# Performance work log

Hardware: AMD Instinct MI355X
Metric: run time of the kernel (lower is better)

The kernel has to match this reference:

```python
import jax, jax.numpy as jnp
import numpy as np

# dims derived from init_kwargs
B, C, T, F = 16, 2, 16, 256
TP, FP = 4, 4            # time/freq patch
MF = F // FP             # 64 freq tokens
TIC = T // TP            # 4 time tokens per chunk
S = MF * TIC             # 256 tokens per chunk
CTX = 3
LEFT = S * CTX           # 768 cached tokens
MT = TIC * (CTX + 1)     # 16 max time positions
D, H, G = 512, 8, 4      # d_model, q heads, kv groups
HD = D // H              # 64
R = H // G               # 2 q-heads per kv group
L = 4                    # layers
FFH = 4 * D
EPS = 1e-5


def _ln(x, g, b):
    m = jnp.mean(x, -1, keepdims=True)
    v = jnp.mean((x - m) ** 2, -1, keepdims=True)
    return (x - m) * jax.lax.rsqrt(v + EPS) * g + b


def setup_inputs() -> dict:
    key = jax.random.key(0)
    ks = iter(jax.random.split(key, 20))
    rn = lambda shape, s=0.05: jax.random.normal(next(ks), shape, jnp.float32) * s
    return {
        "x": rn((B, C, T, F), 1.0),
        "cache_k": rn((L, B, G, LEFT, HD), 1.0),
        "cache_v": rn((L, B, G, LEFT, HD), 1.0),
        "in_W": rn((TP * FP * C, D)), "in_b": jnp.zeros((D,)),
        "ln1_g": jnp.ones((L, D)), "ln1_b": jnp.zeros((L, D)),
        "Wq": rn((L, D, D)), "bq": jnp.zeros((L, D)),
        "Wk": rn((L, D, G * HD)), "bk": jnp.zeros((L, G * HD)),
        "Wv": rn((L, D, G * HD)), "bv": jnp.zeros((L, G * HD)),
        "Wo": rn((L, D, D)), "bo": jnp.zeros((L, D)),
        "rel_time": rn((L, 2 * MT - 1, H)), "rel_freq": rn((L, 2 * MF - 1, H)),
        "res_a": jnp.ones((L,)),
        "ln2_g": jnp.ones((L, D)), "ln2_b": jnp.zeros((L, D)),
        "W1": rn((L, D, FFH)), "b1": jnp.zeros((L, FFH)),
        "W3": rn((L, D, FFH)), "b3": jnp.zeros((L, FFH)),
        "W2": rn((L, FFH, D)), "b2": jnp.zeros((L, D)),
        "res_f": jnp.ones((L,)),
        "out_W": rn((D, TP * FP * C)), "out_b": jnp.zeros((TP * FP * C,)),
    }


def reference(x, cache_k, cache_v, in_W, in_b, ln1_g, ln1_b, Wq, bq, Wk, bk, Wv, bv,
              Wo, bo, rel_time, rel_freq, res_a, ln2_g, ln2_b, W1, b1, W3, b3, W2, b2,
              res_f, out_W, out_b):
    # patchify: (B,C,T,F) -> (B, S, TP*FP*C), token order time-major / freq inner
    h = jnp.transpose(x, (0, 2, 3, 1)).reshape(B, TIC, TP, MF, FP, C)
    h = jnp.transpose(h, (0, 1, 3, 2, 4, 5)).reshape(B, S, TP * FP * C)
    h = h @ in_W + in_b  # (B,S,D)

    # 2D relative position indices (identical each layer)
    K = LEFT + S
    q_idx = jnp.arange(S)
    k_idx = jnp.arange(K)
    qt = LEFT // MF + q_idx // MF  # query time = cache time offset + local time
    qf = q_idx % MF
    kt = k_idx // MF
    kf = k_idx % MF
    dt = qt[:, None] - kt[None, :] + (MT - 1)  # (S,K) in [0, 2*MT-2]
    df = qf[:, None] - kf[None, :] + (MF - 1)  # (S,K) in [0, 2*MF-2]
    scale = 1.0 / np.sqrt(HD).astype(np.float32)

    new_ck, new_cv = [], []
    for l in range(L):
        # --- streaming GQA attention with 2D rel-pos and KV cache ---
        xin = _ln(h, ln1_g[l], ln1_b[l])
        q = (xin @ Wq[l] + bq[l]).reshape(B, S, H, HD)
        k = (xin @ Wk[l] + bk[l]).reshape(B, S, G, HD)
        v = (xin @ Wv[l] + bv[l]).reshape(B, S, G, HD)
        k_full = jnp.concatenate([cache_k[l], jnp.transpose(k, (0, 2, 1, 3))], axis=2)  # (B,G,K,HD)
        v_full = jnp.concatenate([cache_v[l], jnp.transpose(v, (0, 2, 1, 3))], axis=2)
        new_ck.append(k_full[:, :, -LEFT:])
        new_cv.append(v_full[:, :, -LEFT:])
        # group q heads: head h -> group h // R
        scores = jnp.einsum('bsgrd,bgtd->bgrst', q.reshape(B, S, G, R, HD), k_full) * scale
        bias = rel_time[l][dt] + rel_freq[l][df]          # (S,K,H)
        bias = jnp.transpose(bias, (2, 0, 1)).reshape(G, R, S, K)
        attn = jax.nn.softmax(scores + bias[None], axis=-1)
        o = jnp.einsum('bgrst,bgtd->bsgrd', attn, v_full).reshape(B, S, D)
        o = o @ Wo[l] + bo[l]
        h = h + res_a[l] * o  # dropout/droppath identity at eval
        # --- SwiGLU FFN ---
        xin = _ln(h, ln2_g[l], ln2_b[l])
        ff = (jax.nn.silu(xin @ W1[l] + b1[l]) * (xin @ W3[l] + b3[l])) @ W2[l] + b2[l]
        h = h + res_f[l] * ff

    y = h @ out_W + out_b  # (B,S,TP*FP*C)
    # unpatchify back to (B,C,T,F)
    y = y.reshape(B, TIC, MF, TP, FP, C)
    y = jnp.transpose(y, (0, 1, 3, 2, 4, 5)).reshape(B, T, F, C)
    y = jnp.transpose(y, (0, 3, 1, 2))
    return y, jnp.stack(new_ck), jnp.stack(new_cv)
```

## Files before the change

kernel.cpp:

```cpp
#include <hip/hip_runtime.h>
#include <stdint.h>

typedef __attribute__((ext_vector_type(8))) short bf16x8;
typedef __attribute__((ext_vector_type(4))) float f32x4;

#define B_    16
#define S_    256
#define LEFT_ 768
#define KT_   1024
#define D_    512
#define H_    8
#define G_    4
#define HD_   64
#define L_    4
#define FFH_  2048
#define M_    4096
#define LOG2E 1.44269504f

__device__ __forceinline__ unsigned short f2b(float f){
  unsigned u = __float_as_uint(f);
  u += 0x7fffu + ((u>>16)&1u);
  return (unsigned short)(u>>16);
}

__device__ __forceinline__ unsigned cvt_pk_bf16(float lo, float hi){
  unsigned r;
  asm("v_cvt_pk_bf16_f32 %0, %1, %2" : "=v"(r) : "v"(lo), "v"(hi));
  return r;
}

__device__ __forceinline__ void gl_lds16(const unsigned short* g, void* l){
  __builtin_amdgcn_global_load_lds(
    (const __attribute__((address_space(1))) unsigned int*)g,
    (__attribute__((address_space(3))) unsigned int*)l, 16, 0, 0);
}

template<int BM, int BN, int WM, int WN, class BRowF>
__device__ __forceinline__ void mfma_core(
    const unsigned short* Abase, int lda, int m0, BRowF brow,
    int kd, char* As, char* Bs, f32x4* acc)
{
  constexpr int FR = WM/16, FC = WN/16;
  constexpr int NWC = BN/WN;
  constexpr int CA = BM/64, CB = BN/64;
  const int tid = threadIdx.x, wave = tid>>6, lane = tid&63;
  const int wr = wave / NWC, wc = wave % NWC;
  const int lr = lane>>2;
  const int swl = (lane&3) ^ ((lane>>2)&3) ^ (lane>>4);

  auto stage = [&](int buf, int k0){
    #pragma unroll
    for (int i = 0; i < CA; ++i) {
      const int chunk = wave*CA + i;
      const unsigned short* gp = Abase + (size_t)(m0 + chunk*16 + lr)*lda + k0 + swl*8;
      gl_lds16(gp, As + buf*(BM*64) + chunk*1024);
    }
    #pragma unroll
    for (int i = 0; i < CB; ++i) {
      const int chunk = wave*CB + i;
      const unsigned short* gp = brow(chunk*16 + lr) + k0 + swl*8;
      gl_lds16(gp, Bs + buf*(BN*64) + chunk*1024);
    }
  };

  stage(0, 0);
  __syncthreads();
  int cur = 0;
  for (int k0 = 0; k0 < kd; k0 += 32) {
    if (k0 + 32 < kd) stage(cur^1, k0 + 32);
    bf16x8 af[FR], bfr[FC];
    #pragma unroll
    for (int r = 0; r < FR; ++r)
      af[r] = *(const bf16x8*)(As + cur*(BM*64) + (wr*WM + r*16 + (lane&15))*64 + swl*16);
    #pragma unroll
    for (int c = 0; c < FC; ++c)
      bfr[c] = *(const bf16x8*)(Bs + cur*(BN*64) + (wc*WN + c*16 + (lane&15))*64 + swl*16);
    #pragma unroll
    for (int r = 0; r < FR; ++r)
      #pragma unroll
      for (int c = 0; c < FC; ++c)
        acc[r*FC+c] = __builtin_amdgcn_mfma_f32_16x16x32_bf16(af[r], bfr[c], acc[r*FC+c], 0, 0, 0);
    __syncthreads();
    cur ^= 1;
  }
}

__device__ __forceinline__ void tcvt_body(
    const float* __restrict__ src, unsigned short* __restrict__ dst,
    int K, int N, int ntk, int ntn, int bx)
{
  __shared__ float t[64][65];
  int kt = bx % ntk; int nt = (bx/ntk) % ntn; int l = bx/(ntk*ntn);
  src += (size_t)l*K*N; dst += (size_t)l*N*K;
  const int k0 = kt*64, n0 = nt*64;
  const int tid = threadIdx.x;
  #pragma unroll
  for (int i = 0; i < 4; ++i) {
    int kr = (tid>>4) + i*16;
    const float4 v = *(const float4*)&src[(size_t)(k0+kr)*N + n0 + (tid&15)*4];
    t[kr][(tid&15)*4+0]=v.x; t[kr][(tid&15)*4+1]=v.y;
    t[kr][(tid&15)*4+2]=v.z; t[kr][(tid&15)*4+3]=v.w;
  }
  __syncthreads();
  const int nn = tid>>2, kk = (tid&3)*16;
  unsigned w[8];
  #pragma unroll
  for (int j = 0; j < 8; ++j)
    w[j] = (unsigned)f2b(t[kk+2*j][nn]) | ((unsigned)f2b(t[kk+2*j+1][nn])<<16);
  size_t off = (size_t)(n0+nn)*K + k0 + kk;
  *(uint4*)&dst[off]     = make_uint4(w[0],w[1],w[2],w[3]);
  *(uint4*)&dst[off + 8] = make_uint4(w[4],w[5],w[6],w[7]);
}

__global__ __launch_bounds__(256) void transpose_all(
    const float* __restrict__ Wq, const float* __restrict__ Wk,
    const float* __restrict__ Wv, const float* __restrict__ Wo,
    const float* __restrict__ W1, const float* __restrict__ W3,
    const float* __restrict__ W2,
    unsigned short* __restrict__ Wqt, unsigned short* __restrict__ Wkt,
    unsigned short* __restrict__ Wvt, unsigned short* __restrict__ Wot,
    unsigned short* __restrict__ W1t, unsigned short* __restrict__ W3t,
    unsigned short* __restrict__ W2t)
{
  int bx = blockIdx.x;
  if      (bx < 256)  tcvt_body(Wq, Wqt, 512, 512, 8, 8,  bx);
  else if (bx < 384)  tcvt_body(Wk, Wkt, 512, 256, 8, 4,  bx-256);
  else if (bx < 512)  tcvt_body(Wv, Wvt, 512, 256, 8, 4,  bx-384);
  else if (bx < 768)  tcvt_body(Wo, Wot, 512, 512, 8, 8,  bx-512);
  else if (bx < 1792) tcvt_body(W1, W1t, 512, 2048, 8, 32, bx-768);
  else if (bx < 2816) tcvt_body(W3, W3t, 512, 2048, 8, 32, bx-1792);
  else                tcvt_body(W2, W2t, 2048, 512, 32, 8, bx-2816);
}

__global__ __launch_bounds__(256) void patchify_inproj(
    const float* __restrict__ x, const float* __restrict__ inW,
    const float* __restrict__ inb, float* __restrict__ h)
{
  int bs = blockIdx.x;
  int b = bs >> 8, s = bs & 255;
  int tic = s >> 6, mf = s & 63;
  __shared__ float ps[32];
  int tid = threadIdx.x;
  if (tid < 32) {
    int tp = tid >> 3, fp = (tid >> 1) & 3, c = tid & 1;
    ps[tid] = x[((size_t)(b*2 + c)*16 + tic*4 + tp)*256 + mf*4 + fp];
  }
  __syncthreads();
  #pragma unroll
  for (int rep = 0; rep < 2; ++rep) {
    int d = tid + rep*256;
    float acc = inb[d];
    #pragma unroll
    for (int i = 0; i < 32; ++i) acc += ps[i] * inW[i*D_ + d];
    h[(size_t)bs*D_ + d] = acc;
  }
}

__global__ __launch_bounds__(256) void ln_stats(
    const float* __restrict__ h, float* __restrict__ smean, float* __restrict__ srstd)
{
  const int tid = threadIdx.x;
  const int row = blockIdx.x*16 + (tid>>4);
  const int qd = tid & 15;
  const float* rp = h + (size_t)row*512 + qd*32;
  float s = 0.f, sq = 0.f;
  #pragma unroll
  for (int i = 0; i < 8; ++i) {
    float4 v = ((const float4*)rp)[i];
    s  += (v.x+v.y)+(v.z+v.w);
    sq += (v.x*v.x+v.y*v.y)+(v.z*v.z+v.w*v.w);
  }
  #pragma unroll
  for (int o = 1; o < 16; o <<= 1) { s += __shfl_xor(s,o,64); sq += __shfl_xor(sq,o,64); }
  if (qd == 0) {
    float mean = s*(1.f/512.f);
    smean[row] = mean;
    srstd[row] = rsqrtf(sq*(1.f/512.f) - mean*mean + 1e-5f);
  }
}

__global__ __launch_bounds__(256) void ln_kernel(
    const float* __restrict__ in, unsigned short* __restrict__ out,
    const float* __restrict__ g, const float* __restrict__ bta)
{
  const int tid = threadIdx.x;
  const int row = blockIdx.x*16 + (tid>>4);
  const int qd = tid & 15;
  const float* rp = in + (size_t)row*512 + qd*32;
  float4 xv[8];
  float s = 0.f, sq = 0.f;
  #pragma unroll
  for (int i = 0; i < 8; ++i) {
    xv[i] = ((const float4*)rp)[i];
    s  += (xv[i].x+xv[i].y)+(xv[i].z+xv[i].w);
    sq += (xv[i].x*xv[i].x + xv[i].y*xv[i].y)+(xv[i].z*xv[i].z + xv[i].w*xv[i].w);
  }
  #pragma unroll
  for (int o = 1; o < 16; o <<= 1) { s += __shfl_xor(s,o,64); sq += __shfl_xor(sq,o,64); }
  const float mean = s*(1.f/512.f);
  const float rstd = rsqrtf(sq*(1.f/512.f) - mean*mean + 1e-5f);
  const float* gp = g + qd*32;
  const float* bp = bta + qd*32;
  unsigned short* op = out + (size_t)row*512 + qd*32;
  #pragma unroll
  for (int i = 0; i < 4; ++i) {
    float4 a  = xv[2*i],                 b2 = xv[2*i+1];
    float4 ga = ((const float4*)gp)[2*i], gb = ((const float4*)gp)[2*i+1];
    float4 ba = ((const float4*)bp)[2*i], bb = ((const float4*)bp)[2*i+1];
    unsigned w0 = (unsigned)f2b((a.x-mean)*rstd*ga.x + ba.x) | ((unsigned)f2b((a.y-mean)*rstd*ga.y + ba.y)<<16);
    unsigned w1 = (unsigned)f2b((a.z-mean)*rstd*ga.z + ba.z) | ((unsigned)f2b((a.w-mean)*rstd*ga.w + ba.w)<<16);
    unsigned w2 = (unsigned)f2b((b2.x-mean)*rstd*gb.x + bb.x) | ((unsigned)f2b((b2.y-mean)*rstd*gb.y + bb.y)<<16);
    unsigned w3 = (unsigned)f2b((b2.z-mean)*rstd*gb.z + bb.z) | ((unsigned)f2b((b2.w-mean)*rstd*gb.w + bb.w)<<16);
    *(uint4*)(op + i*8) = make_uint4(w0,w1,w2,w3);
  }
}

__global__ __launch_bounds__(256) void qkv_ln_gemm(
    const float* __restrict__ h,
    const float* __restrict__ smean, const float* __restrict__ srstd,
    const float* __restrict__ lng, const float* __restrict__ lnb,
    const unsigned short* __restrict__ Wqt, const unsigned short* __restrict__ Wkt,
    const unsigned short* __restrict__ Wvt,
    const float* __restrict__ bq, const float* __restrict__ bk_, const float* __restrict__ bv_,
    unsigned short* __restrict__ q_bf, unsigned short* __restrict__ kf_bf,
    unsigned short* __restrict__ vnew, float* __restrict__ nck, float* __restrict__ ncv)
{
  __shared__ alignas(16) char As[2][64*64];
  __shared__ alignas(16) char Bs[2][128*64];
  int bx = (blockIdx.x & 7)*64 + (blockIdx.x >> 3);
  const int mt = bx >> 3, nt = bx & 7;
  const int m0 = mt*64, n0 = nt*128;
  const int tid = threadIdx.x, wave = tid>>6, lane = tid&63;

  const int ar = tid >> 2, au = tid & 3;
  const int ap = au ^ (ar&3) ^ ((ar>>2)&3);
  const float* arow = h + (size_t)(m0 + ar)*512;
  const float mean_r = smean[m0 + ar];
  const float rstd_r = srstd[m0 + ar];

  const int lr = lane>>2;
  const int swl = (lane&3) ^ ((lane>>2)&3) ^ (lane>>4);
  auto brow = [&](int rr) -> const unsigned short* {
    int n = n0 + rr;
    return n < 512 ? Wqt + (size_t)n*512
         : n < 768 ? Wkt + (size_t)(n-512)*512
                   : Wvt + (size_t)(n-768)*512;
  };
  auto stageB = [&](int buf, int k0){
    #pragma unroll
    for (int i = 0; i < 2; ++i) {
      const int chunk = wave*2 + i;
      gl_lds16(brow(chunk*16+lr) + k0 + swl*8, (char*)Bs[buf] + chunk*1024);
    }
  };

  float4 av[6];
  auto loadA = [&](int k0){
    av[0] = *(const float4*)(arow + k0 + au*8);
    av[1] = *(const float4*)(arow + k0 + au*8 + 4);
    av[2] = *(const float4*)(lng  + k0 + au*8);
    av[3] = *(const float4*)(lng  + k0 + au*8 + 4);
    av[4] = *(const float4*)(lnb  + k0 + au*8);
    av[5] = *(const float4*)(lnb  + k0 + au*8 + 4);
  };
  auto writeA = [&](int buf){
    const float* xv = (const float*)&av[0];
    const float* gv = (const float*)&av[2];
    const float* bv2 = (const float*)&av[4];
    unsigned w[4];
    #pragma unroll
    for (int j = 0; j < 4; ++j) {
      float e0 = (xv[2*j]   - mean_r)*rstd_r*gv[2*j]   + bv2[2*j];
      float e1 = (xv[2*j+1] - mean_r)*rstd_r*gv[2*j+1] + bv2[2*j+1];
      w[j] = (unsigned)f2b(e0) | ((unsigned)f2b(e1)<<16);
    }
    *(uint4*)((char*)As[buf] + ar*64 + ap*16) = make_uint4(w[0],w[1],w[2],w[3]);
  };

  loadA(0);
  stageB(0, 0);
  writeA(0);
  __syncthreads();

  f32x4 acc[8] = {};
  const int wr = wave >> 1, wc = wave & 1;
  for (int k0 = 0; k0 < 512; k0 += 32) {
    const int cur = (k0>>5)&1;
    const bool more = (k0 + 32 < 512);
    if (more) { stageB(cur^1, k0+32); loadA(k0+32); }
    bf16x8 af[2], bfv[4];
    #pragma unroll
    for (int r = 0; r < 2; ++r)
      af[r] = *(const bf16x8*)((char*)As[cur] + (wr*32 + r*16 + (lane&15))*64 + swl*16);
    #pragma unroll
    for (int c = 0; c < 4; ++c)
      bfv[c] = *(const bf16x8*)((char*)Bs[cur] + (wc*64 + c*16 + (lane&15))*64 + swl*16);
    #pragma unroll
    for (int r = 0; r < 2; ++r)
      #pragma unroll
      for (int c = 0; c < 4; ++c)
        acc[r*4+c] = __builtin_amdgcn_mfma_f32_16x16x32_bf16(af[r], bfv[c], acc[r*4+c], 0,0,0);
    if (more) writeA(cur^1);
    __syncthreads();
  }

  #pragma unroll
  for (int r = 0; r < 2; ++r)
  #pragma unroll
  for (int c = 0; c < 4; ++c) {
    f32x4 v = acc[r*4+c];
    #pragma unroll
    for (int reg = 0; reg < 4; ++reg) {
      int m = m0 + wr*32 + r*16 + ((lane>>4)<<2) + reg;
      int n = n0 + wc*64 + c*16 + (lane&15);
      float val = v[reg];
      int b = m >> 8, s = m & 255;
      if (n < 512) {
        q_bf[(size_t)m*512 + n] = f2b(val + bq[n]);
      } else if (n < 768) {
        int g = (n-512) >> 6, hd = n & 63;
        float kv = val + bk_[n-512];
        kf_bf[((size_t)(b*4+g)*1024 + 768 + s)*64 + hd] = f2b(kv);
        nck [((size_t)(b*4+g)*768  + 512 + s)*64 + hd] = kv;
      } else {
        int g = (n-768) >> 6, hd = n & 63;
        float vv = val + bv_[n-768];
        vnew[(size_t)m*256 + (n-768)] = f2b(vv);
        ncv [((size_t)(b*4+g)*768 + 512 + s)*64 + hd] = vv;
      }
    }
  }
}

__global__ __launch_bounds__(256) void merge_kv(
    const float* __restrict__ ck, const float* __restrict__ cv,
    const unsigned short* __restrict__ vnew,
    unsigned short* __restrict__ kf_bf, unsigned short* __restrict__ vt_bf,
    float* __restrict__ nck, float* __restrict__ ncv)
{
  __shared__ float t[64][65];
  const int bb = blockIdx.x;
  const int tid = threadIdx.x;
  if (bb < 3072) {
    size_t idx = (size_t)bb*256 + tid;
    int hd4 = idx & 15;
    size_t tt = (idx >> 4) % 768;
    size_t bg = idx / (16*768);
    const float4 v = ((const float4*)ck)[idx];
    uint2 pk;
    pk.x = (unsigned)f2b(v.x) | ((unsigned)f2b(v.y)<<16);
    pk.y = (unsigned)f2b(v.z) | ((unsigned)f2b(v.w)<<16);
    *(uint2*)&kf_bf[((bg*1024 + tt)*64) + hd4*4] = pk;
    if (tt >= 256)
      ((float4*)nck)[(bg*768 + (tt-256))*16 + hd4] = v;
  } else if (bb < 3840) {
    const int bi = bb - 3072;
    const int bg = bi / 12, tt = bi % 12;
    const int t0 = tt*64;
    #pragma unroll
    for (int i = 0; i < 4; ++i) {
      int tr = (tid>>4) + i*16;
      const float4 v = ((const float4*)cv)[((size_t)bg*768 + t0+tr)*16 + (tid&15)];
      t[tr][(tid&15)*4+0]=v.x; t[tr][(tid&15)*4+1]=v.y;
      t[tr][(tid&15)*4+2]=v.z; t[tr][(tid&15)*4+3]=v.w;
      if (t0+tr >= 256)
        ((float4*)ncv)[((size_t)bg*768 + t0+tr-256)*16 + (tid&15)] = v;
    }
    __syncthreads();
    const int hd = tid>>2, tc = (tid&3)*16;
    unsigned w[8];
    #pragma unroll
    for (int j = 0; j < 8; ++j)
      w[j] = (unsigned)f2b(t[tc+2*j][hd]) | ((unsigned)f2b(t[tc+2*j+1][hd])<<16);
    size_t off = ((size_t)bg*64 + hd)*1024 + t0 + tc;
    *(uint4*)&vt_bf[off]     = make_uint4(w[0],w[1],w[2],w[3]);
    *(uint4*)&vt_bf[off + 8] = make_uint4(w[4],w[5],w[6],w[7]);
  } else {
    const int bi = bb - 3840;
    const int bg = bi >> 2, tt4 = bi & 3;
    const int b = bg >> 2, g = bg & 3;
    const int t0 = 768 + tt4*64;
    unsigned short* ts = (unsigned short*)&t[0][0];
    #pragma unroll
    for (int i = 0; i < 4; ++i) {
      int tr = (tid>>4) + i*16;
      uint2 v = *(const uint2*)&vnew[((size_t)(b*256 + (t0-768) + tr))*256 + g*64 + (tid&15)*4];
      const unsigned short* pv4 = (const unsigned short*)&v;
      ts[tr*68 + (tid&15)*4 + 0] = pv4[0];
      ts[tr*68 + (tid&15)*4 + 1] = pv4[1];
      ts[tr*68 + (tid&15)*4 + 2] = pv4[2];
      ts[tr*68 + (tid&15)*4 + 3] = pv4[3];
    }
    __syncthreads();
    const int hd = tid>>2, tc = (tid&3)*16;
    unsigned w[8];
    #pragma unroll
    for (int j = 0; j < 8; ++j)
      w[j] = (unsigned)ts[(tc+2*j)*68 + hd] | ((unsigned)ts[(tc+2*j+1)*68 + hd] << 16);
    size_t off = ((size_t)bg*64 + hd)*1024 + t0 + tc;
    *(uint4*)&vt_bf[off]     = make_uint4(w[0],w[1],w[2],w[3]);
    *(uint4*)&vt_bf[off + 8] = make_uint4(w[4],w[5],w[6],w[7]);
  }
}

__global__ __launch_bounds__(512) void flash_attn(
    const unsigned short* __restrict__ q_bf,
    const unsigned short* __restrict__ kf_bf,
    const unsigned short* __restrict__ vt_bf,
    const float* __restrict__ relt,
    const float* __restrict__ relf,
    unsigned short* __restrict__ att_bf)
{
  int bx = (blockIdx.x & 7)*32 + (blockIdx.x >> 3);
  const int qt = bx & 1, hh = (bx>>1) & 7, b = bx >> 4;
  const int g = hh >> 1;
  const int tid = threadIdx.x, wave = tid>>6, lane = tid&63;
  const int lg = lane>>4, lq = lane&15;
  const int qloc = wave*16 + lq;
  const int q0 = qt*128;
  const int qtg = qt*2 + (wave>>2);

  __shared__ alignas(16) char Ks[2][16384];
  __shared__ alignas(16) char Vs[2][16384];

  const unsigned short* kfb  = kf_bf + (size_t)(b*4+g)*1024*64;
  const unsigned short* vtb2 = vt_bf + (size_t)(b*4+g)*64*1024;

  auto stage = [&](int buf, int t){
    #pragma unroll
    for (int it = 0; it < 2; ++it) {
      int slot = it*512 + tid;
      int kr = slot>>3, kp = slot&7,  ku = kp ^ (kr&7);
      gl_lds16(kfb + (size_t)(t*128 + kr)*64 + ku*8, Ks[buf] + slot*16);
      int vr = slot>>4, vp = slot&15, vu = vp ^ (vr&15);
      gl_lds16(vtb2 + (size_t)vr*1024 + t*128 + vu*8, Vs[buf] + slot*16);
    }
  };

  const unsigned short* qrow = q_bf + ((size_t)(b*256 + q0 + qloc))*512 + hh*64;
  bf16x8 qfrag[2];
  qfrag[0] = *(const bf16x8*)(qrow + lg*8);
  qfrag[1] = *(const bf16x8*)(qrow + 32 + lg*8);

  float bias_f[4][4];
  {
    int sq = qloc & 63;
    #pragma unroll
    for (int f = 0; f < 4; ++f)
      #pragma unroll
      for (int r = 0; r < 4; ++r)
        bias_f[f][r] = relf[((sq - (f*16 + lg*4 + r)) + 63)*8 + hh] * LOG2E;
  }
  const float scale2 = 0.125f * LOG2E;

  f32x4 ot[4] = {};
  float m_run = -1e30f, l_part = 0.f;

  stage(0, 0);
  __syncthreads();

  for (int t = 0; t < 8; ++t) {
    const int cur = t & 1;
    if (t + 1 < 8) stage(cur^1, t+1);

    f32x4 st[8] = {};
    __builtin_amdgcn_s_setprio(1);
    #pragma unroll
    for (int c = 0; c < 2; ++c)
      #pragma unroll
      for (int f = 0; f < 8; ++f) {
        int row = f*16 + lq;
        int pu = (c*4 + lg) ^ (row & 7);
        bf16x8 kf_ = *(const bf16x8*)(Ks[cur] + row*128 + pu*16);
        st[f] = __builtin_amdgcn_mfma_f32_16x16x32_bf16(kf_, qfrag[c], st[f], 0,0,0);
      }
    __builtin_amdgcn_s_setprio(0);

    const float bt0 = relt[(27 + qtg - 2*t)*8 + hh] * LOG2E;
    const float bt1 = relt[(27 + qtg - 2*t - 1)*8 + hh] * LOG2E;
    float mt = -1e30f;
    #pragma unroll
    for (int f = 0; f < 8; ++f) {
      const float bt = (f < 4) ? bt0 : bt1;
      #pragma unroll
      for (int r = 0; r < 4; ++r) {
        float v = st[f][r]*scale2 + bt + bias_f[f&3][r];
        st[f][r] = v;
        mt = fmaxf(mt, v);
      }
    }
    mt = fmaxf(mt, __shfl_xor(mt, 16, 64));
    mt = fmaxf(mt, __shfl_xor(mt, 32, 64));
    if (!__all(mt - m_run <= 11.5416f)) {
      const float m_new = fmaxf(m_run, mt);
      const float corr = exp2f(m_run - m_new);
      m_run = m_new;
      l_part *= corr;
      #pragma unroll
      for (int f = 0; f < 4; ++f) {
        ot[f][0] *= corr; ot[f][1] *= corr; ot[f][2] *= corr; ot[f][3] *= corr;
      }
    }
    float psum = 0.f;
    unsigned r01[8], r23[8];
    #pragma unroll
    for (int f = 0; f < 8; ++f) {
      float e0 = exp2f(st[f][0] - m_run);
      float e1 = exp2f(st[f][1] - m_run);
      float e2 = exp2f(st[f][2] - m_run);
      float e3 = exp2f(st[f][3] - m_run);
      psum += (e0+e1)+(e2+e3);
      r01[f] = cvt_pk_bf16(e0, e1);
      r23[f] = cvt_pk_bf16(e2, e3);
    }
    l_part += psum;

    const int src0 = (lg&1)*32 + lq;
    const int src1 = src0 + 16;
    const bool hi = (lg>>1) != 0;
    #pragma unroll
    for (int c = 0; c < 4; ++c) {
      unsigned a0 = (unsigned)__shfl((int)r01[c*2],   src0, 64);
      unsigned b0 = (unsigned)__shfl((int)r01[c*2+1], src0, 64);
      unsigned a1 = (unsigned)__shfl((int)r23[c*2],   src0, 64);
      unsigned b1 = (unsigned)__shfl((int)r23[c*2+1], src0, 64);
      unsigned a2 = (unsigned)__shfl((int)r01[c*2],   src1, 64);
      unsigned b2 = (unsigned)__shfl((int)r01[c*2+1], src1, 64);
      unsigned a3 = (unsigned)__shfl((int)r23[c*2],   src1, 64);
      unsigned b3 = (unsigned)__shfl((int)r23[c*2+1], src1, 64);
      uint4 bw;
      bw.x = hi ? b0 : a0;
      bw.y = hi ? b1 : a1;
      bw.z = hi ? b2 : a2;
      bw.w = hi ? b3 : a3;
      bf16x8 pfrag = *(bf16x8*)&bw;
      __builtin_amdgcn_s_setprio(1);
      #pragma unroll
      for (int f = 0; f < 4; ++f) {
        int row = f*16 + lq;
        int pu = (c*4 + lg) ^ (row & 15);
        bf16x8 vf_ = *(const bf16x8*)(Vs[cur] + row*256 + pu*16);
        ot[f] = __builtin_amdgcn_mfma_f32_16x16x32_bf16(vf_, pfrag, ot[f], 0,0,0);
      }
      __builtin_amdgcn_s_setprio(0);
    }
    __syncthreads();
  }

  float l_tot = l_part + __shfl_xor(l_part, 16, 64);
  l_tot += __shfl_xor(l_tot, 32, 64);
  const float inv = 1.0f / l_tot;
  unsigned short* orow = att_bf + ((size_t)(b*256 + q0 + qloc))*512 + hh*64;
  #pragma unroll
  for (int f = 0; f < 4; ++f) {
    uint2 w;
    w.x = (unsigned)f2b(ot[f][0]*inv) | ((unsigned)f2b(ot[f][1]*inv)<<16);
    w.y = (unsigned)f2b(ot[f][2]*inv) | ((unsigned)f2b(ot[f][3]*inv)<<16);
    *(uint2*)(orow + f*16 + lg*4) = w;
  }
}

__global__ __launch_bounds__(256) void ffn1_gemm(
    const unsigned short* __restrict__ xin,
    const unsigned short* __restrict__ W1t, const unsigned short* __restrict__ W3t,
    const float* __restrict__ b1_, const float* __restrict__ b3_,
    unsigned short* __restrict__ ff_bf)
{
  __shared__ alignas(16) char As[2*128*64];
  __shared__ alignas(16) char Bs[2*128*64];
  f32x4 acc[16] = {};
  int bx = (blockIdx.x & 7)*128 + (blockIdx.x >> 3);
  const int nt = bx & 31, mt = bx >> 5;
  const int m0 = mt*128, n0 = nt*128;
  auto brow = [&](int r) -> const unsigned short* {
    int p = n0 + r;
    int pb = p >> 4;
    int j = ((pb>>1)<<4) | (p & 15);
    return (pb & 1) ? W3t + (size_t)j*512 : W1t + (size_t)j*512;
  };
  mfma_core<128,128,64,64>(xin, 512, m0, brow, 512, As, Bs, acc);
  const int lane = threadIdx.x & 63, wave = threadIdx.x >> 6;
  const int wr = wave >> 1, wc = wave & 1;
  #pragma unroll
  for (int r = 0; r < 4; ++r)
  #pragma unroll
  for (int cp = 0; cp < 4; cp += 2) {
    f32x4 va = acc[r*4+cp];
    f32x4 vb = acc[r*4+cp+1];
    #pragma unroll
    for (int reg = 0; reg < 4; ++reg) {
      int m = m0 + wr*64 + r*16 + ((lane>>4)<<2) + reg;
      int p = n0 + wc*64 + cp*16 + (lane&15);
      int j = ((p>>5)<<4) | (p & 15);
      float a = va[reg] + b1_[j];
      float bb = vb[reg] + b3_[j];
      float gval = (a / (1.0f + __expf(-a))) * bb;
      ff_bf[(size_t)m*2048 + j] = f2b(gval);
    }
  }
}

__global__ __launch_bounds__(256) void res_gemm(
    const unsigned short* __restrict__ A, int lda,
    const unsigned short* __restrict__ Wt, int kd,
    const float* __restrict__ bias, const float* __restrict__ resv,
    float* __restrict__ h)
{
  __shared__ alignas(16) char As[2*64*64];
  __shared__ alignas(16) char Bs[2*64*64];
  f32x4 acc[4] = {};
  int bx = (blockIdx.x & 7)*64 + (blockIdx.x >> 3);
  const int mt = bx >> 3, nt = bx & 7;
  const int m0 = mt*64, n0 = nt*64;
  auto brow = [&](int r) -> const unsigned short* {
    return Wt + (size_t)(n0 + r)*kd;
  };
  mfma_core<64,64,32,32>(A, lda, m0, brow, kd, As, Bs, acc);
  const float rv = resv[0];
  const int lane = threadIdx.x & 63, wave = threadIdx.x >> 6;
  const int wr = wave >> 1, wc = wave & 1;
  #pragma unroll
  for (int r = 0; r < 2; ++r)
  #pragma unroll
  for (int c = 0; c < 2; ++c) {
    f32x4 v = acc[r*2+c];
    #pragma unroll
    for (int reg = 0; reg < 4; ++reg) {
      int m = m0 + wr*32 + r*16 + ((lane>>4)<<2) + reg;
      int n = n0 + wc*32 + c*16 + (lane&15);
      h[(size_t)m*512 + n] += rv * (v[reg] + bias[n]);
    }
  }
}

__global__ __launch_bounds__(256) void outproj_kernel(
    const float* __restrict__ h, const float* __restrict__ outW,
    const float* __restrict__ outb, float* __restrict__ y)
{
  int bs = blockIdx.x;
  int b = bs >> 8, s = bs & 255;
  int tic = s >> 6, mf = s & 63;
  __shared__ float hr[512];
  __shared__ float part[8][32];
  int tid = threadIdx.x;
  hr[tid]     = h[(size_t)bs*D_ + tid];
  hr[tid+256] = h[(size_t)bs*D_ + tid + 256];
  __syncthreads();
  int i = tid & 31, seg = tid >> 5;
  float acc = 0.0f;
  #pragma unroll
  for (int k = 0; k < 64; ++k) acc += hr[seg*64 + k] * outW[(seg*64 + k)*32 + i];
  part[seg][i] = acc;
  __syncthreads();
  if (tid < 32) {
    float v = outb[tid];
    #pragma unroll
    for (int s2 = 0; s2 < 8; ++s2) v += part[s2][tid];
    int tp = tid >> 3, fp = (tid >> 1) & 3, c = tid & 1;
    y[((size_t)(b*2 + c)*16 + tic*4 + tp)*256 + mf*4 + fp] = v;
  }
}

extern "C" void kernel_launch(void* const* d_in, const int* in_sizes, int n_in,
                              void* d_out, int out_size, void* d_ws, size_t ws_size,
                              hipStream_t stream) {
  (void)in_sizes; (void)n_in; (void)out_size; (void)ws_size;
  const float* x        = (const float*)d_in[0];
  const float* cache_k  = (const float*)d_in[1];
  const float* cache_v  = (const float*)d_in[2];
  const float* in_W     = (const float*)d_in[3];
  const float* in_b     = (const float*)d_in[4];
  const float* ln1_g    = (const float*)d_in[5];
  const float* ln1_b    = (const float*)d_in[6];
  const float* Wq       = (const float*)d_in[7];
  const float* bq       = (const float*)d_in[8];
  const float* Wk       = (const float*)d_in[9];
  const float* bk       = (const float*)d_in[10];
  const float* Wv       = (const float*)d_in[11];
  const float* bv       = (const float*)d_in[12];
  const float* Wo       = (const float*)d_in[13];
  const float* bo       = (const float*)d_in[14];
  const float* rel_time = (const float*)d_in[15];
  const float* rel_freq = (const float*)d_in[16];
  const float* res_a    = (const float*)d_in[17];
  const float* ln2_g    = (const float*)d_in[18];
  const float* ln2_b    = (const float*)d_in[19];
  const float* W1       = (const float*)d_in[20];
  const float* b1       = (const float*)d_in[21];
  const float* W3       = (const float*)d_in[22];
  const float* b3       = (const float*)d_in[23];
  const float* W2       = (const float*)d_in[24];
  const float* b2       = (const float*)d_in[25];
  const float* res_f    = (const float*)d_in[26];
  const float* out_W    = (const float*)d_in[27];
  const float* out_b    = (const float*)d_in[28];

  char* ws = (char*)d_ws;
  size_t o = 0;
  float* h            = (float*)(ws + o);          o += (size_t)4096*512*4;
  unsigned short* xin = (unsigned short*)(ws + o); o += (size_t)4096*512*2;
  unsigned short* qb  = (unsigned short*)(ws + o); o += (size_t)4096*512*2;
  unsigned short* att = (unsigned short*)(ws + o); o += (size_t)4096*512*2;
  unsigned short* kfb = (unsigned short*)(ws + o); o += (size_t)64*1024*64*2;
  unsigned short* vtb = (unsigned short*)(ws + o); o += (size_t)64*64*1024*2;
  unsigned short* vnw = (unsigned short*)(ws + o); o += (size_t)4096*256*2;
  float* smean        = (float*)(ws + o);          o += (size_t)4096*4;
  float* srstd        = (float*)(ws + o);          o += (size_t)4096*4;
  unsigned short* Wqt = (unsigned short*)(ws + o); o += (size_t)4*512*512*2;
  unsigned short* Wkt = (unsigned short*)(ws + o); o += (size_t)4*256*512*2;
  unsigned short* Wvt = (unsigned short*)(ws + o); o += (size_t)4*256*512*2;
  unsigned short* Wot = (unsigned short*)(ws + o); o += (size_t)4*512*512*2;
  unsigned short* W1t = (unsigned short*)(ws + o); o += (size_t)4*2048*512*2;
  unsigned short* W3t = (unsigned short*)(ws + o); o += (size_t)4*2048*512*2;
  unsigned short* W2t = (unsigned short*)(ws + o); o += (size_t)4*512*2048*2;
  unsigned short* ffb = (unsigned short*)(ws + o);

  float* y    = (float*)d_out;
  float* nck0 = y + 131072;
  float* ncv0 = nck0 + 12582912;

  transpose_all<<<3840, 256, 0, stream>>>(Wq, Wk, Wv, Wo, W1, W3, W2,
                                          Wqt, Wkt, Wvt, Wot, W1t, W3t, W2t);

  patchify_inproj<<<M_, 256, 0, stream>>>(x, in_W, in_b, h);

  for (int l = 0; l < L_; ++l) {
    ln_stats<<<256, 256, 0, stream>>>(h, smean, srstd);
    qkv_ln_gemm<<<512, 256, 0, stream>>>(
        h, smean, srstd, ln1_g + l*512, ln1_b + l*512,
        Wqt + (size_t)l*512*512, Wkt + (size_t)l*256*512, Wvt + (size_t)l*256*512,
        bq + l*512, bk + l*256, bv + l*256,
        qb, kfb, vnw, nck0 + (size_t)l*3145728, ncv0 + (size_t)l*3145728);
    merge_kv<<<4096, 256, 0, stream>>>(
        cache_k + (size_t)l*3145728, cache_v + (size_t)l*3145728, vnw,
        kfb, vtb, nck0 + (size_t)l*3145728, ncv0 + (size_t)l*3145728);
    flash_attn<<<256, 512, 0, stream>>>(qb, kfb, vtb,
        rel_time + l*31*8, rel_freq + l*127*8, att);
    res_gemm<<<512, 256, 0, stream>>>(att, 512, Wot + (size_t)l*512*512, 512,
                                      bo + l*512, res_a + l, h);
    ln_kernel<<<256, 256, 0, stream>>>(h, xin, ln2_g + l*512, ln2_b + l*512);
    ffn1_gemm<<<1024, 256, 0, stream>>>(
        xin, W1t + (size_t)l*2048*512, W3t + (size_t)l*2048*512,
        b1 + l*2048, b3 + l*2048, ffb);
    res_gemm<<<512, 256, 0, stream>>>(ffb, 2048, W2t + (size_t)l*512*2048, 2048,
                                      b2 + l*512, res_f + l, h);
  }

  outproj_kernel<<<M_, 256, 0, stream>>>(h, out_W, out_b, y);
}
```

Before: 614.8 us.

## Batch patchify tokens with LDS-staged weights, custom pipelined res_gemm, software bf16 pack

```diff
diff --git a/kernel.cpp b/kernel.cpp
--- a/kernel.cpp
+++ b/kernel.cpp
@@ -23,12 +23,6 @@
   return (unsigned short)(u>>16);
 }
 
-__device__ __forceinline__ unsigned cvt_pk_bf16(float lo, float hi){
-  unsigned r;
-  asm("v_cvt_pk_bf16_f32 %0, %1, %2" : "=v"(r) : "v"(lo), "v"(hi));
-  return r;
-}
-
 __device__ __forceinline__ void gl_lds16(const unsigned short* g, void* l){
   __builtin_amdgcn_global_load_lds(
     (const __attribute__((address_space(1))) unsigned int*)g,
@@ -136,23 +130,37 @@
     const float* __restrict__ x, const float* __restrict__ inW,
     const float* __restrict__ inb, float* __restrict__ h)
 {
-  int bs = blockIdx.x;
-  int b = bs >> 8, s = bs & 255;
-  int tic = s >> 6, mf = s & 63;
-  __shared__ float ps[32];
-  int tid = threadIdx.x;
-  if (tid < 32) {
-    int tp = tid >> 3, fp = (tid >> 1) & 3, c = tid & 1;
-    ps[tid] = x[((size_t)(b*2 + c)*16 + tic*4 + tp)*256 + mf*4 + fp];
+  __shared__ float wlds[32*512];
+  __shared__ float ps[16][33];
+  const int tid = threadIdx.x;
+  const int tb = blockIdx.x*16;
+
+  #pragma unroll
+  for (int i = 0; i < 16; ++i)
+    ((float4*)wlds)[i*256 + tid] = ((const float4*)inW)[i*256 + tid];
+  {
+    int tok = tid >> 5, idx = tid & 31;
+    int bs = tb + tok;
+    int b = bs >> 8, s = bs & 255;
+    int tic = s >> 6, mf = s & 63;
+    int tp = idx >> 3, fp = (idx >> 1) & 3, c = idx & 1;
+    ps[tok][idx] = x[((size_t)(b*2 + c)*16 + tic*4 + tp)*256 + mf*4 + fp];
+    int tok2 = tok + 8;
+    int bs2 = tb + tok2;
+    int b2 = bs2 >> 8, s2 = bs2 & 255;
+    int tic2 = s2 >> 6, mf2 = s2 & 63;
+    ps[tok2][idx] = x[((size_t)(b2*2 + c)*16 + tic2*4 + tp)*256 + mf2*4 + fp];
   }
   __syncthreads();
-  #pragma unroll
-  for (int rep = 0; rep < 2; ++rep) {
-    int d = tid + rep*256;
+
+  const int g = tid >> 4, qd = tid & 15;
+  const int bs = tb + g;
+  for (int j = 0; j < 32; ++j) {
+    int d = j*16 + qd;
     float acc = inb[d];
     #pragma unroll
-    for (int i = 0; i < 32; ++i) acc += ps[i] * inW[i*D_ + d];
-    h[(size_t)bs*D_ + d] = acc;
+    for (int i = 0; i < 32; ++i) acc += ps[g][i] * wlds[i*512 + d];
+    h[(size_t)bs*512 + d] = acc;
   }
 }
 
@@ -510,8 +518,8 @@
       float e2 = exp2f(st[f][2] - m_run);
       float e3 = exp2f(st[f][3] - m_run);
       psum += (e0+e1)+(e2+e3);
-      r01[f] = cvt_pk_bf16(e0, e1);
-      r23[f] = cvt_pk_bf16(e2, e3);
+      r01[f] = (unsigned)f2b(e0) | ((unsigned)f2b(e1)<<16);
+      r23[f] = (unsigned)f2b(e2) | ((unsigned)f2b(e3)<<16);
     }
     l_part += psum;
 
@@ -606,19 +614,50 @@
     const float* __restrict__ bias, const float* __restrict__ resv,
     float* __restrict__ h)
 {
-  __shared__ alignas(16) char As[2*64*64];
-  __shared__ alignas(16) char Bs[2*64*64];
+  __shared__ alignas(16) char As[4][64*64];
+  __shared__ alignas(16) char Bs[4][64*64];
   f32x4 acc[4] = {};
   int bx = (blockIdx.x & 7)*64 + (blockIdx.x >> 3);
   const int mt = bx >> 3, nt = bx & 7;
   const int m0 = mt*64, n0 = nt*64;
-  auto brow = [&](int r) -> const unsigned short* {
-    return Wt + (size_t)(n0 + r)*kd;
+  const int tid = threadIdx.x, wave = tid>>6, lane = tid&63;
+  const int wr = wave >> 1, wc = wave & 1;
+  const int lr = lane>>2;
+  const int swl = (lane&3) ^ ((lane>>2)&3) ^ (lane>>4);
+
+  auto stageP = [&](int slot, int k0){
+    gl_lds16(A  + (size_t)(m0 + wave*16 + lr)*lda + k0 + swl*8, As[slot] + wave*1024);
+    gl_lds16(Wt + (size_t)(n0 + wave*16 + lr)*kd  + k0 + swl*8, Bs[slot] + wave*1024);
   };
-  mfma_core<64,64,32,32>(A, lda, m0, brow, kd, As, Bs, acc);
+
+  stageP(0, 0);
+  stageP(1, 32);
+  __syncthreads();
+  int cur = 0;
+  for (int k0 = 0; k0 < kd; k0 += 64) {
+    if (k0 + 64 < kd) { stageP((cur^1)*2, k0+64); stageP((cur^1)*2+1, k0+96); }
+    #pragma unroll
+    for (int p = 0; p < 2; ++p) {
+      const char* ab = As[cur*2+p];
+      const char* bb = Bs[cur*2+p];
+      bf16x8 af[2], bfv[2];
+      #pragma unroll
+      for (int r = 0; r < 2; ++r)
+        af[r] = *(const bf16x8*)(ab + (wr*32 + r*16 + (lane&15))*64 + swl*16);
+      #pragma unroll
+      for (int c = 0; c < 2; ++c)
+        bfv[c] = *(const bf16x8*)(bb + (wc*32 + c*16 + (lane&15))*64 + swl*16);
+      #pragma unroll
+      for (int r = 0; r < 2; ++r)
+        #pragma unroll
+        for (int c = 0; c < 2; ++c)
+          acc[r*2+c] = __builtin_amdgcn_mfma_f32_16x16x32_bf16(af[r], bfv[c], acc[r*2+c], 0,0,0);
+    }
+    __syncthreads();
+    cur ^= 1;
+  }
+
   const float rv = resv[0];
-  const int lane = threadIdx.x & 63, wave = threadIdx.x >> 6;
-  const int wr = wave >> 1, wc = wave & 1;
   #pragma unroll
   for (int r = 0; r < 2; ++r)
   #pragma unroll
@@ -722,7 +761,7 @@
   transpose_all<<<3840, 256, 0, stream>>>(Wq, Wk, Wv, Wo, W1, W3, W2,
                                           Wqt, Wkt, Wvt, Wot, W1t, W3t, W2t);
 
-  patchify_inproj<<<M_, 256, 0, stream>>>(x, in_W, in_b, h);
+  patchify_inproj<<<256, 256, 0, stream>>>(x, in_W, in_b, h);
 
   for (int l = 0; l < L_; ++l) {
     ln_stats<<<256, 256, 0, stream>>>(h, smean, srstd);
```

After: 602.3 us (median of 2 runs). 2.0% less time.
